# Kernel tuning notes

Measured on AMD Instinct MI355X. Metric: run time of the kernel, lower is better.

Reference implementation:

```python
import jax, jax.numpy as jnp
import numpy as np

B, N, K, M = 4, 32768, 128, 1024
C_IN, C_OUT, C_ATT, H = 256, 256, 256, 8
G = 32  # GroupNorm groups
EPS = 1e-6


def heat_diffusion(x, mass, evals, evecs, t):
    # to_basis: evecs^T @ (mass * x)  -> [B,K,C]
    x_spec = jnp.einsum('bnk,bnc->bkc', evecs, x * mass[..., None])
    coefs = jnp.exp(-evals[..., None] * t[None, None, :])  # [B,K,C]
    # from_basis: evecs @ spec -> [B,N,C]
    return jnp.einsum('bnk,bkc->bnc', evecs, coefs * x_spec)


def setup_inputs() -> dict:
    key = jax.random.key(0)
    ks = jax.random.split(key, 16)
    x = jax.random.normal(ks[0], (B, N, C_IN), jnp.float32)
    mass = jax.random.uniform(ks[1], (B, N), jnp.float32, 0.1, 1.0)
    evals = jnp.sort(jax.random.uniform(ks[2], (B, K), jnp.float32, 0.0, 10.0), axis=-1)
    evecs = jax.random.normal(ks[3], (B, N, K), jnp.float32) / np.sqrt(N)
    # unique sorted farthest-point indices per mesh (equiv. to boolean mask with M True)
    far_idx = jnp.stack([jnp.sort(jax.random.permutation(jax.random.fold_in(ks[4], b), N)[:M])
                         for b in range(B)]).astype(jnp.int32)
    s = 1.0 / np.sqrt(C_IN)
    params = dict(
        diff_in_t=jnp.full((C_IN,), 0.01, jnp.float32),
        diff_out_t=jnp.full((C_OUT,), 0.01, jnp.float32),
        gn_w=jnp.ones((C_IN,), jnp.float32),
        gn_b=jnp.zeros((C_IN,), jnp.float32),
        Wq=jax.random.normal(ks[5], (C_IN, C_ATT), jnp.float32) * s,
        bq=jnp.zeros((C_ATT,), jnp.float32),
        Wk=jax.random.normal(ks[6], (C_IN, C_ATT), jnp.float32) * s,
        bk=jnp.zeros((C_ATT,), jnp.float32),
        Wv=jax.random.normal(ks[7], (C_IN, C_ATT), jnp.float32) * s,
        bv=jnp.zeros((C_ATT,), jnp.float32),
        Wo=jax.random.normal(ks[8], (C_ATT, C_OUT), jnp.float32) * s,
        bo=jnp.zeros((C_OUT,), jnp.float32),
        out_w=jnp.ones((C_OUT,), jnp.float32),
    )
    return dict(x=x, mass=mass, evals=evals, evecs=evecs, far_idx=far_idx, **params)


def reference(x, mass, evals, evecs, far_idx, diff_in_t, diff_out_t, gn_w, gn_b,
              Wq, bq, Wk, bk, Wv, bv, Wo, bo, out_w):
    # clamp (torch does this in-place under no_grad)
    diff_in_t = jnp.maximum(diff_in_t, 1e-8)
    diff_out_t = jnp.maximum(diff_out_t, 1e-8)
    out_w = jnp.maximum(out_w, 1e-8)

    x = heat_diffusion(x, mass, evals, evecs, diff_in_t)  # [B,N,C_IN]

    # masked gather of farthest points -> [B,M,C_IN]
    x_far = jnp.take_along_axis(x, far_idx[..., None], axis=1)

    # GroupNorm over (group-channels, points)
    xg = x_far.reshape(B, M, G, C_IN // G)
    mu = jnp.mean(xg, axis=(1, 3), keepdims=True)
    var = jnp.var(xg, axis=(1, 3), keepdims=True)
    xg = (xg - mu) * jax.lax.rsqrt(var + EPS)
    x_far = xg.reshape(B, M, C_IN) * gn_w + gn_b

    d = C_ATT // H
    q = (x_far @ Wq + bq).reshape(B, M, H, d)
    k = (x_far @ Wk + bk).reshape(B, M, H, d)
    v = (x_far @ Wv + bv).reshape(B, M, H, d)
    scores = jnp.einsum('bqhd,bkhd->bhqk', q, k) / np.sqrt(d)
    attn = jax.nn.softmax(scores, axis=-1)
    x_far = jnp.einsum('bhqk,bkhd->bqhd', attn, v).reshape(B, M, C_ATT)
    x_far = x_far @ Wo + bo  # [B,M,C_OUT]

    # scatter back into zeros at the farthest-point rows
    z = jnp.zeros((B, N, C_OUT), x.dtype)
    z = z.at[jnp.arange(B)[:, None], far_idx].set(x_far)

    out = heat_diffusion(z, mass, evals, evecs, diff_out_t)
    return out * out_w[None, None, :]
```

## Files before the change

kernel.cpp:

```cpp
#include <hip/hip_runtime.h>
#include <hip/hip_bf16.h>


#define Bn 4
#define Nn 32768
#define Kn 128
#define Cn 256
#define Mn 1024
#define Hn 8
#define Dn 32
#define NCH 64
#define MCH 16
#define SEG 8

typedef _Float16 f16;
typedef _Float16 f16x8 __attribute__((ext_vector_type(8)));
typedef float f32x4 __attribute__((ext_vector_type(4)));

__device__ __forceinline__ void gload_lds16(const float* g, float* l) {
    __builtin_amdgcn_global_load_lds(
        (const __attribute__((address_space(1))) void*)g,
        (__attribute__((address_space(3))) void*)l, 16, 0, 0);
}

__global__ __launch_bounds__(512) void k_tobasis1(
    const float* __restrict__ x, const float* __restrict__ mass,
    const float* __restrict__ evecs, float* __restrict__ part)
{
    const int nch = blockIdx.x, b = blockIdx.z;
    const int n0 = nch * (Nn / NCH);
    const int t = threadIdx.x;
    const int lane = t & 63, w = t >> 6;
    const int lr = lane & 15, lg = lane >> 4;
    const int wm = (w & 1) * 64;
    const int wc = (w >> 1) * 64;

    __shared__ float evS[32][128];
    __shared__ float xS[32][256];
    __shared__ __align__(16) f16 evH[128][40];
    __shared__ __align__(16) f16 evL[128][40];
    __shared__ __align__(16) f16 xH[256][40];
    __shared__ __align__(16) f16 xL[256][40];

    const size_t rb0 = (size_t)b * Nn + n0;

    f32x4 acc[4][4] = {};

    {
        const float* eb = evecs + rb0 * Kn;
        const float* xb = x + rb0 * Cn;
#pragma unroll
        for (int iw = 0; iw < 2; iw++) {
            const int sl = w * 2 + iw;
            gload_lds16(eb + sl * 256 + lane * 4, (float*)evS + sl * 256);
        }
#pragma unroll
        for (int iw = 0; iw < 4; iw++) {
            const int sl = w * 4 + iw;
            gload_lds16(xb + sl * 256 + lane * 4, (float*)xS + sl * 256);
        }
    }

    for (int s = 0; s < 16; s++) {
        asm volatile("s_waitcnt vmcnt(0)" ::: "memory");
        __builtin_amdgcn_s_barrier();

        {
            const int k = (w & 1) * 64 + lane;
            const int g = w >> 1;
            f16x8 hv, lv;
#pragma unroll
            for (int r = 0; r < 8; r++) {
                const float f = evS[g * 8 + r][k];
                const f16 h = (f16)f;
                hv[r] = h;
                lv[r] = (f16)(f - (float)h);
            }
            *(f16x8*)&evH[k][g * 8] = hv;
            *(f16x8*)&evL[k][g * 8] = lv;
        }
#pragma unroll
        for (int i = 0; i < 2; i++) {
            const int c = (w & 3) * 64 + lane;
            const int g = i * 2 + (w >> 2);
            const size_t rowb = rb0 + s * 32 + g * 8;
            f16x8 hv, lv;
#pragma unroll
            for (int r = 0; r < 8; r++) {
                const float f = xS[g * 8 + r][c] * mass[rowb + r];
                const f16 h = (f16)f;
                hv[r] = h;
                lv[r] = (f16)(f - (float)h);
            }
            *(f16x8*)&xH[c][g * 8] = hv;
            *(f16x8*)&xL[c][g * 8] = lv;
        }

        asm volatile("s_waitcnt lgkmcnt(0)" ::: "memory");
        __builtin_amdgcn_s_barrier();

        if (s < 15) {
            const float* eb = evecs + (rb0 + (size_t)(s + 1) * 32) * Kn;
            const float* xb = x + (rb0 + (size_t)(s + 1) * 32) * Cn;
#pragma unroll
            for (int iw = 0; iw < 2; iw++) {
                const int sl = w * 2 + iw;
                gload_lds16(eb + sl * 256 + lane * 4, (float*)evS + sl * 256);
            }
#pragma unroll
            for (int iw = 0; iw < 4; iw++) {
                const int sl = w * 4 + iw;
                gload_lds16(xb + sl * 256 + lane * 4, (float*)xS + sl * 256);
            }
        }

        f16x8 aH[4], aL[4], bH[4], bL[4];
#pragma unroll
        for (int i = 0; i < 4; i++) {
            aH[i] = *(const f16x8*)&evH[wm + i * 16 + lr][lg * 8];
            aL[i] = *(const f16x8*)&evL[wm + i * 16 + lr][lg * 8];
            bH[i] = *(const f16x8*)&xH[wc + i * 16 + lr][lg * 8];
            bL[i] = *(const f16x8*)&xL[wc + i * 16 + lr][lg * 8];
        }
#pragma unroll
        for (int i = 0; i < 4; i++)
#pragma unroll
            for (int j = 0; j < 4; j++) {
                acc[i][j] = __builtin_amdgcn_mfma_f32_16x16x32_f16(aH[i], bH[j], acc[i][j], 0, 0, 0);
                acc[i][j] = __builtin_amdgcn_mfma_f32_16x16x32_f16(aH[i], bL[j], acc[i][j], 0, 0, 0);
                acc[i][j] = __builtin_amdgcn_mfma_f32_16x16x32_f16(aL[i], bH[j], acc[i][j], 0, 0, 0);
            }
    }

    float* dst = part + ((size_t)b * NCH + nch) * (Kn * Cn);
#pragma unroll
    for (int i = 0; i < 4; i++)
#pragma unroll
        for (int j = 0; j < 4; j++) {
            const int m0 = wm + i * 16 + lg * 4;
            const int c = wc + j * 16 + lr;
#pragma unroll
            for (int r = 0; r < 4; r++)
                dst[(size_t)(m0 + r) * Cn + c] = acc[i][j][r];
        }
}

__global__ __launch_bounds__(256) void k_reduce(
    const float* __restrict__ part, int nchunks,
    const float* __restrict__ evals, const float* __restrict__ tvec,
    float* __restrict__ spec)
{
    const int b = blockIdx.x >> 7, k = blockIdx.x & 127, c = threadIdx.x;
    float ssum = 0.f;
    const float* p = part + ((size_t)b * nchunks * Kn + k) * Cn + c;
    for (int j = 0; j < nchunks; j++) ssum += p[(size_t)j * Kn * Cn];
    const float lam = evals[b * Kn + k];
    const float tt = fmaxf(tvec[c], 1e-8f);
    spec[((size_t)b * Kn + k) * Cn + c] = ssum * __expf(-lam * tt);
}

__global__ __launch_bounds__(128) void k_gather(
    const float* __restrict__ evecs, const float* __restrict__ mass,
    const int* __restrict__ far, float* __restrict__ evf, float* __restrict__ massf)
{
    const int row = blockIdx.x;
    const int b = row >> 10;
    const int idx = far[row];
    const int t = threadIdx.x;
    evf[(size_t)row * Kn + t] = evecs[((size_t)b * Nn + idx) * Kn + t];
    if (t == 0) massf[row] = mass[(size_t)b * Nn + idx];
}

struct G3 {
    const float* W[3];
    const float* bias[3];
    float* out[3];
};

template<int KD, bool PERB, bool MMASS>
__global__ __launch_bounds__(256) void k_gemm64(
    const float* __restrict__ X, G3 g, const float* __restrict__ massf)
{
    const int mt = blockIdx.x, ct = blockIdx.y, z = blockIdx.z;
    const int row0 = mt * 64, c0 = ct * 64;
    const int b = row0 >> 10;
    const float* Wp = g.W[z];
    const float* bias = g.bias[z];
    float* out = g.out[z];
    const size_t woff = PERB ? (size_t)b * KD * 256 : 0;

    __shared__ float xT[32][68];
    __shared__ float wl[32][64];
    const int t = threadIdx.x, tx = t & 15, ty = t >> 4;
    float acc[4][4] = {};

    for (int k0 = 0; k0 < KD; k0 += 32) {
        {
            const int m = t >> 2, cc0 = (t & 3) * 8;
            const float* xs = X + (size_t)(row0 + m) * KD + k0 + cc0;
            float4 a0 = *(const float4*)xs, a1 = *(const float4*)(xs + 4);
            xT[cc0 + 0][m] = a0.x; xT[cc0 + 1][m] = a0.y; xT[cc0 + 2][m] = a0.z; xT[cc0 + 3][m] = a0.w;
            xT[cc0 + 4][m] = a1.x; xT[cc0 + 5][m] = a1.y; xT[cc0 + 6][m] = a1.z; xT[cc0 + 7][m] = a1.w;
        }
        {
            const int cc = t >> 3, col = (t & 7) * 8;
            const float* wsrc = Wp + woff + (size_t)(k0 + cc) * 256 + c0 + col;
            float4 a0 = *(const float4*)wsrc, a1 = *(const float4*)(wsrc + 4);
            wl[cc][col + 0] = a0.x; wl[cc][col + 1] = a0.y; wl[cc][col + 2] = a0.z; wl[cc][col + 3] = a0.w;
            wl[cc][col + 4] = a1.x; wl[cc][col + 5] = a1.y; wl[cc][col + 6] = a1.z; wl[cc][col + 7] = a1.w;
        }
        __syncthreads();
#pragma unroll 8
        for (int cc = 0; cc < 32; cc++) {
            float4 xv = *(const float4*)&xT[cc][ty * 4];
            float4 wv = *(const float4*)&wl[cc][tx * 4];
            float xa[4] = {xv.x, xv.y, xv.z, xv.w};
            float wa[4] = {wv.x, wv.y, wv.z, wv.w};
#pragma unroll
            for (int i = 0; i < 4; i++)
#pragma unroll
                for (int j = 0; j < 4; j++) acc[i][j] += xa[i] * wa[j];
        }
        __syncthreads();
    }
    float bj[4] = {0.f, 0.f, 0.f, 0.f};
    if (bias) {
#pragma unroll
        for (int j = 0; j < 4; j++) bj[j] = bias[c0 + tx * 4 + j];
    }
#pragma unroll
    for (int i = 0; i < 4; i++) {
        const int row = row0 + ty * 4 + i;
        const float mm = MMASS ? massf[row] : 1.f;
        *(float4*)(out + (size_t)row * 256 + c0 + tx * 4) =
            make_float4((acc[i][0] + bj[0]) * mm, (acc[i][1] + bj[1]) * mm,
                        (acc[i][2] + bj[2]) * mm, (acc[i][3] + bj[3]) * mm);
    }
}

__global__ __launch_bounds__(256) void k_gnstats(const float* __restrict__ xfar, float* __restrict__ gst)
{
    const int b = blockIdx.x >> 5, g = blockIdx.x & 31;
    const int t = threadIdx.x;
    float s = 0.f, s2 = 0.f;
#pragma unroll
    for (int i = 0; i < 4; i++) {
        const int m = t * 4 + i;
        const float* p = xfar + ((size_t)b * Mn + m) * Cn + g * 8;
        float4 a = *(const float4*)p;
        float4 c = *(const float4*)(p + 4);
        s += a.x + a.y + a.z + a.w + c.x + c.y + c.z + c.w;
        s2 += a.x * a.x + a.y * a.y + a.z * a.z + a.w * a.w +
              c.x * c.x + c.y * c.y + c.z * c.z + c.w * c.w;
    }
    __shared__ float sb[256], sb2[256];
    sb[t] = s; sb2[t] = s2;
    __syncthreads();
    for (int o = 128; o > 0; o >>= 1) {
        if (t < o) { sb[t] += sb[t + o]; sb2[t] += sb2[t + o]; }
        __syncthreads();
    }
    if (t == 0) {
        const float mean = sb[0] * (1.f / 8192.f);
        const float var = sb2[0] * (1.f / 8192.f) - mean * mean;
        gst[2 * blockIdx.x] = mean;
        gst[2 * blockIdx.x + 1] = rsqrtf(var + 1e-6f);
    }
}

__global__ __launch_bounds__(256) void k_gnapply(
    const float* __restrict__ xfar, const float* __restrict__ gst,
    const float* __restrict__ gw, const float* __restrict__ gb, float* __restrict__ xn)
{
    const int idx = (blockIdx.x * 256 + threadIdx.x) * 4;
    const int c = idx & 255;
    const int row = idx >> 8;
    const int b = row >> 10;
    const int g = c >> 3;
    const float2 st = *(const float2*)&gst[2 * (b * 32 + g)];
    float4 vv = *(const float4*)&xfar[idx];
    float4 w4 = *(const float4*)&gw[c];
    float4 b4 = *(const float4*)&gb[c];
    float4 o;
    o.x = (vv.x - st.x) * st.y * w4.x + b4.x;
    o.y = (vv.y - st.x) * st.y * w4.y + b4.y;
    o.z = (vv.z - st.x) * st.y * w4.z + b4.z;
    o.w = (vv.w - st.x) * st.y * w4.w + b4.w;
    *(float4*)&xn[idx] = o;
}

__global__ __launch_bounds__(256) void k_attn(
    const float* __restrict__ q, const float* __restrict__ kbuf, const float* __restrict__ vbuf,
    float* __restrict__ pacc, float* __restrict__ pm, float* __restrict__ pl)
{
    const int qt = blockIdx.x;
    const int seg = blockIdx.y;
    const int bh = blockIdx.z;
    const int b = bh >> 3, h = bh & 7;
    const int t = threadIdx.x;
    const int tx = t & 15, ty = t >> 4;

    __shared__ float qT[32][68];
    __shared__ float kT[32][68];
    __shared__ float vsm[64][36];
    __shared__ float psT[64][72];
    __shared__ float red[64][16];

    const int q0 = qt * 64;
    {
        const int row = t >> 2, d0 = (t & 3) * 8;
        const float* qp = q + ((size_t)b * Mn + q0 + row) * Cn + h * Dn + d0;
        float4 a0 = *(const float4*)qp, a1 = *(const float4*)(qp + 4);
        qT[d0 + 0][row] = a0.x; qT[d0 + 1][row] = a0.y; qT[d0 + 2][row] = a0.z; qT[d0 + 3][row] = a0.w;
        qT[d0 + 4][row] = a1.x; qT[d0 + 5][row] = a1.y; qT[d0 + 6][row] = a1.z; qT[d0 + 7][row] = a1.w;
    }

    const float scale = 0.17677669529663687f;
    float m_i[4], l_i[4], acc[4][2];
#pragma unroll
    for (int i = 0; i < 4; i++) { m_i[i] = -1e30f; l_i[i] = 0.f; acc[i][0] = 0.f; acc[i][1] = 0.f; }

    for (int kt = 0; kt < 2; kt++) {
        __syncthreads();
        {
            const int row = t >> 2, d0 = (t & 3) * 8;
            const int k0 = seg * 128 + kt * 64;
            const float* kp = kbuf + ((size_t)b * Mn + k0 + row) * Cn + h * Dn + d0;
            float4 a0 = *(const float4*)kp, a1 = *(const float4*)(kp + 4);
            kT[d0 + 0][row] = a0.x; kT[d0 + 1][row] = a0.y; kT[d0 + 2][row] = a0.z; kT[d0 + 3][row] = a0.w;
            kT[d0 + 4][row] = a1.x; kT[d0 + 5][row] = a1.y; kT[d0 + 6][row] = a1.z; kT[d0 + 7][row] = a1.w;
            const float* vp = vbuf + ((size_t)b * Mn + k0 + row) * Cn + h * Dn + d0;
            *(float4*)&vsm[row][d0] = *(const float4*)vp;
            *(float4*)&vsm[row][d0 + 4] = *(const float4*)(vp + 4);
        }
        __syncthreads();

        float s[4][4] = {};
#pragma unroll 8
        for (int d = 0; d < 32; d++) {
            float4 qv = *(const float4*)&qT[d][ty * 4];
            float4 kv = *(const float4*)&kT[d][tx * 4];
            float qa[4] = {qv.x, qv.y, qv.z, qv.w};
            float ka[4] = {kv.x, kv.y, kv.z, kv.w};
#pragma unroll
            for (int i = 0; i < 4; i++)
#pragma unroll
                for (int j = 0; j < 4; j++) s[i][j] += qa[i] * ka[j];
        }
        float tmax[4];
#pragma unroll
        for (int i = 0; i < 4; i++) {
            s[i][0] *= scale; s[i][1] *= scale; s[i][2] *= scale; s[i][3] *= scale;
            tmax[i] = fmaxf(fmaxf(s[i][0], s[i][1]), fmaxf(s[i][2], s[i][3]));
        }
#pragma unroll
        for (int i = 0; i < 4; i++) red[ty * 4 + i][tx] = tmax[i];
        __syncthreads();
        float nm[4];
#pragma unroll
        for (int i = 0; i < 4; i++) {
            const int row = ty * 4 + i;
            float mx = m_i[i];
#pragma unroll
            for (int xj = 0; xj < 16; xj++) mx = fmaxf(mx, red[row][xj]);
            nm[i] = mx;
        }
        __syncthreads();
        float tsum[4];
#pragma unroll
        for (int i = 0; i < 4; i++) {
            float p0 = __expf(s[i][0] - nm[i]);
            float p1 = __expf(s[i][1] - nm[i]);
            float p2 = __expf(s[i][2] - nm[i]);
            float p3 = __expf(s[i][3] - nm[i]);
            s[i][0] = p0; s[i][1] = p1; s[i][2] = p2; s[i][3] = p3;
            tsum[i] = p0 + p1 + p2 + p3;
        }
#pragma unroll
        for (int kk = 0; kk < 4; kk++)
            *(float4*)&psT[tx * 4 + kk][ty * 4] = make_float4(s[0][kk], s[1][kk], s[2][kk], s[3][kk]);
#pragma unroll
        for (int i = 0; i < 4; i++) red[ty * 4 + i][tx] = tsum[i];
        __syncthreads();
#pragma unroll
        for (int i = 0; i < 4; i++) {
            const int row = ty * 4 + i;
            float rs = 0.f;
#pragma unroll
            for (int xj = 0; xj < 16; xj++) rs += red[row][xj];
            const float r = __expf(m_i[i] - nm[i]);
            l_i[i] = l_i[i] * r + rs;
            m_i[i] = nm[i];
            acc[i][0] *= r; acc[i][1] *= r;
        }
#pragma unroll 8
        for (int k = 0; k < 64; k++) {
            float4 pv = *(const float4*)&psT[k][ty * 4];
            float2 vv = *(const float2*)&vsm[k][tx * 2];
            acc[0][0] += pv.x * vv.x; acc[0][1] += pv.x * vv.y;
            acc[1][0] += pv.y * vv.x; acc[1][1] += pv.y * vv.y;
            acc[2][0] += pv.z * vv.x; acc[2][1] += pv.z * vv.y;
            acc[3][0] += pv.w * vv.x; acc[3][1] += pv.w * vv.y;
        }
    }
#pragma unroll
    for (int i = 0; i < 4; i++) {
        const int m = q0 + ty * 4 + i;
        const size_t pr = (((size_t)seg * Bn + b) * Hn + h) * Mn + m;
        if (tx == 0) { pm[pr] = m_i[i]; pl[pr] = l_i[i]; }
        *(float2*)(pacc + pr * 32 + tx * 2) = make_float2(acc[i][0], acc[i][1]);
    }
}

__global__ __launch_bounds__(256) void k_comb(
    const float* __restrict__ pacc, const float* __restrict__ pm, const float* __restrict__ pl,
    float* __restrict__ att)
{
    const int t = threadIdx.x;
    const size_t row = (size_t)blockIdx.x * 8 + (t >> 5);
    const int j = t & 31;
    float M = -1e30f;
#pragma unroll
    for (int s = 0; s < SEG; s++) M = fmaxf(M, pm[(size_t)s * 32768 + row]);
    float L = 0.f, a = 0.f;
#pragma unroll
    for (int s = 0; s < SEG; s++) {
        const float w = __expf(pm[(size_t)s * 32768 + row] - M);
        L += w * pl[(size_t)s * 32768 + row];
        a += w * pacc[((size_t)s * 32768 + row) * 32 + j];
    }
    const int bh = (int)(row >> 10);
    const int mrow = (int)(row & 1023);
    const int b = bh >> 3, h = bh & 7;
    att[((size_t)b * Mn + mrow) * Cn + h * 32 + j] = a / L;
}

__global__ __launch_bounds__(256) void k_tobasis2(
    const float* __restrict__ evf, const float* __restrict__ xo, float* __restrict__ part)
{
    const int mch = blockIdx.x, ct = blockIdx.y, b = blockIdx.z;
    const int m0 = mch * (Mn / MCH);
    const int c0 = ct * 128;
    __shared__ float ev[32][128];
    __shared__ float xm[32][128];
    const int t = threadIdx.x, tx = t & 15, ty = t >> 4;
    float acc[8][8];
#pragma unroll
    for (int i = 0; i < 8; i++)
#pragma unroll
        for (int j = 0; j < 8; j++) acc[i][j] = 0.f;
    const int lr = t >> 3, lc = (t & 7) * 16;
    for (int s = 0; s < Mn / MCH; s += 32) {
        const size_t mrow = (size_t)b * Mn + m0 + s + lr;
        {
            const float* es = evf + mrow * Kn + lc;
            *(float4*)&ev[lr][lc]      = *(const float4*)es;
            *(float4*)&ev[lr][lc + 4]  = *(const float4*)(es + 4);
            *(float4*)&ev[lr][lc + 8]  = *(const float4*)(es + 8);
            *(float4*)&ev[lr][lc + 12] = *(const float4*)(es + 12);
            const float* xs = xo + mrow * Cn + c0 + lc;
            *(float4*)&xm[lr][lc]      = *(const float4*)xs;
            *(float4*)&xm[lr][lc + 4]  = *(const float4*)(xs + 4);
            *(float4*)&xm[lr][lc + 8]  = *(const float4*)(xs + 8);
            *(float4*)&xm[lr][lc + 12] = *(const float4*)(xs + 12);
        }
        __syncthreads();
#pragma unroll 4
        for (int nn = 0; nn < 32; nn++) {
            float4 e0 = *(const float4*)&ev[nn][ty * 4];
            float4 e1 = *(const float4*)&ev[nn][64 + ty * 4];
            float4 x0 = *(const float4*)&xm[nn][tx * 4];
            float4 x1 = *(const float4*)&xm[nn][64 + tx * 4];
            float ee[8] = {e0.x, e0.y, e0.z, e0.w, e1.x, e1.y, e1.z, e1.w};
            float xx[8] = {x0.x, x0.y, x0.z, x0.w, x1.x, x1.y, x1.z, x1.w};
#pragma unroll
            for (int i = 0; i < 8; i++)
#pragma unroll
                for (int j = 0; j < 8; j++) acc[i][j] += ee[i] * xx[j];
        }
        __syncthreads();
    }
    float* dst = part + ((size_t)b * MCH + mch) * (Kn * Cn);
#pragma unroll
    for (int i = 0; i < 8; i++) {
        const int k = (i < 4) ? (ty * 4 + i) : (64 + ty * 4 + i - 4);
        *(float4*)(dst + (size_t)k * Cn + c0 + tx * 4) =
            make_float4(acc[i][0], acc[i][1], acc[i][2], acc[i][3]);
        *(float4*)(dst + (size_t)k * Cn + c0 + 64 + tx * 4) =
            make_float4(acc[i][4], acc[i][5], acc[i][6], acc[i][7]);
    }
}

__global__ __launch_bounds__(256) void k_frombasis2(
    const float* __restrict__ evecs, const float* __restrict__ spec,
    const float* __restrict__ outw, float* __restrict__ out)
{
    const int nt = blockIdx.x, ct = blockIdx.y, b = blockIdx.z;
    const int n0 = nt * 128, c0 = ct * 128;
    __shared__ float evT[32][132];
    __shared__ float sp[32][128];
    const int t = threadIdx.x, tx = t & 15, ty = t >> 4;
    float acc[8][8];
#pragma unroll
    for (int i = 0; i < 8; i++)
#pragma unroll
        for (int j = 0; j < 8; j++) acc[i][j] = 0.f;
    const int en = t >> 1, ek0 = (t & 1) * 16;
    const int sr = t >> 3, sc = (t & 7) * 16;
    for (int k0 = 0; k0 < Kn; k0 += 32) {
        {
            const float* es = evecs + ((size_t)b * Nn + n0 + en) * Kn + k0 + ek0;
            float4 a0 = *(const float4*)es, a1 = *(const float4*)(es + 4);
            float4 a2 = *(const float4*)(es + 8), a3 = *(const float4*)(es + 12);
            evT[ek0 + 0][en] = a0.x; evT[ek0 + 1][en] = a0.y; evT[ek0 + 2][en] = a0.z; evT[ek0 + 3][en] = a0.w;
            evT[ek0 + 4][en] = a1.x; evT[ek0 + 5][en] = a1.y; evT[ek0 + 6][en] = a1.z; evT[ek0 + 7][en] = a1.w;
            evT[ek0 + 8][en] = a2.x; evT[ek0 + 9][en] = a2.y; evT[ek0 + 10][en] = a2.z; evT[ek0 + 11][en] = a2.w;
            evT[ek0 + 12][en] = a3.x; evT[ek0 + 13][en] = a3.y; evT[ek0 + 14][en] = a3.z; evT[ek0 + 15][en] = a3.w;
            const float* ss = spec + ((size_t)b * Kn + k0 + sr) * Cn + c0 + sc;
            *(float4*)&sp[sr][sc]      = *(const float4*)ss;
            *(float4*)&sp[sr][sc + 4]  = *(const float4*)(ss + 4);
            *(float4*)&sp[sr][sc + 8]  = *(const float4*)(ss + 8);
            *(float4*)&sp[sr][sc + 12] = *(const float4*)(ss + 12);
        }
        __syncthreads();
#pragma unroll 4
        for (int kk2 = 0; kk2 < 32; kk2++) {
            float4 e0 = *(const float4*)&evT[kk2][ty * 4];
            float4 e1 = *(const float4*)&evT[kk2][64 + ty * 4];
            float4 s0 = *(const float4*)&sp[kk2][tx * 4];
            float4 s1 = *(const float4*)&sp[kk2][64 + tx * 4];
            float ee[8] = {e0.x, e0.y, e0.z, e0.w, e1.x, e1.y, e1.z, e1.w};
            float sv[8] = {s0.x, s0.y, s0.z, s0.w, s1.x, s1.y, s1.z, s1.w};
#pragma unroll
            for (int i = 0; i < 8; i++)
#pragma unroll
                for (int j = 0; j < 8; j++) acc[i][j] += ee[i] * sv[j];
        }
        __syncthreads();
    }
    float ow[8];
#pragma unroll
    for (int j = 0; j < 8; j++) {
        const int c = c0 + ((j < 4) ? (tx * 4 + j) : (64 + tx * 4 + j - 4));
        ow[j] = fmaxf(outw[c], 1e-8f);
    }
#pragma unroll
    for (int i = 0; i < 8; i++) {
        const int n = n0 + ((i < 4) ? (ty * 4 + i) : (64 + ty * 4 + i - 4));
        float* od = out + ((size_t)b * Nn + n) * Cn + c0;
        *(float4*)(od + tx * 4) =
            make_float4(acc[i][0] * ow[0], acc[i][1] * ow[1], acc[i][2] * ow[2], acc[i][3] * ow[3]);
        *(float4*)(od + 64 + tx * 4) =
            make_float4(acc[i][4] * ow[4], acc[i][5] * ow[5], acc[i][6] * ow[6], acc[i][7] * ow[7]);
    }
}

extern "C" void kernel_launch(void* const* d_in, const int* in_sizes, int n_in,
                              void* d_out, int out_size, void* d_ws, size_t ws_size,
                              hipStream_t stream)
{
    const float* x     = (const float*)d_in[0];
    const float* mass  = (const float*)d_in[1];
    const float* evals = (const float*)d_in[2];
    const float* evecs = (const float*)d_in[3];
    const int*   far   = (const int*)d_in[4];
    const float* t_in  = (const float*)d_in[5];
    const float* t_out = (const float*)d_in[6];
    const float* gn_w  = (const float*)d_in[7];
    const float* gn_b  = (const float*)d_in[8];
    const float* Wq    = (const float*)d_in[9];
    const float* bq    = (const float*)d_in[10];
    const float* Wk    = (const float*)d_in[11];
    const float* bk    = (const float*)d_in[12];
    const float* Wv    = (const float*)d_in[13];
    const float* bv    = (const float*)d_in[14];
    const float* Wo    = (const float*)d_in[15];
    const float* bo    = (const float*)d_in[16];
    const float* outw  = (const float*)d_in[17];
    float* out = (float*)d_out;
    float* ws = (float*)d_ws;

    float* A     = ws;
    float* evf   = ws    + 8388608;
    float* massf = evf   + 524288;
    float* gst   = massf + 4096;
    float* pm    = gst   + 256;
    float* pl    = pm    + 262144;
    float* spec1 = pl    + 262144;
    float* xfar  = spec1 + 131072;
    float* xn    = xfar  + 1048576;
    float* q     = xn    + 1048576;
    float* kk    = q     + 1048576;
    float* v     = kk    + 1048576;
    float* pacc  = A;
    float* part2 = A;
    float* spec2 = spec1;
    float* xo    = xfar;
    float* att   = xn;

    k_tobasis1<<<dim3(NCH, 1, Bn), 512, 0, stream>>>(x, mass, evecs, A);
    k_reduce<<<Bn * Kn, Cn, 0, stream>>>(A, NCH, evals, t_in, spec1);
    k_gather<<<Bn * Mn, Kn, 0, stream>>>(evecs, mass, far, evf, massf);
    {
        G3 g{};
        g.W[0] = spec1; g.bias[0] = nullptr; g.out[0] = xfar;
        k_gemm64<128, true, false><<<dim3(64, 4, 1), 256, 0, stream>>>(evf, g, nullptr);
    }
    k_gnstats<<<Bn * 32, 256, 0, stream>>>(xfar, gst);
    k_gnapply<<<1024, 256, 0, stream>>>(xfar, gst, gn_w, gn_b, xn);
    {
        G3 g{};
        g.W[0] = Wq; g.W[1] = Wk; g.W[2] = Wv;
        g.bias[0] = bq; g.bias[1] = bk; g.bias[2] = bv;
        g.out[0] = q; g.out[1] = kk; g.out[2] = v;
        k_gemm64<256, false, false><<<dim3(64, 4, 3), 256, 0, stream>>>(xn, g, nullptr);
    }
    k_attn<<<dim3(16, SEG, 32), 256, 0, stream>>>(q, kk, v, pacc, pm, pl);
    k_comb<<<4096, 256, 0, stream>>>(pacc, pm, pl, att);
    {
        G3 g{};
        g.W[0] = Wo; g.bias[0] = bo; g.out[0] = xo;
        k_gemm64<256, false, true><<<dim3(64, 4, 1), 256, 0, stream>>>(att, g, massf);
    }
    k_tobasis2<<<dim3(MCH, 2, Bn), 256, 0, stream>>>(evf, xo, part2);
    k_reduce<<<Bn * Kn, Cn, 0, stream>>>(part2, MCH, evals, t_out, spec2);
    k_frombasis2<<<dim3(256, 2, Bn), 256, 0, stream>>>(evecs, spec2, outw, out);
}
```

Measured before the change: 628.9 us.

## Double-buffer staging in to-basis kernel, swizzle f16 split tiles, stage mass in LDS

```diff
diff --git a/kernel.cpp b/kernel.cpp
--- a/kernel.cpp
+++ b/kernel.cpp
@@ -35,92 +35,96 @@
     const int wm = (w & 1) * 64;
     const int wc = (w >> 1) * 64;
 
-    __shared__ float evS[32][128];
-    __shared__ float xS[32][256];
-    __shared__ __align__(16) f16 evH[128][40];
-    __shared__ __align__(16) f16 evL[128][40];
-    __shared__ __align__(16) f16 xH[256][40];
-    __shared__ __align__(16) f16 xL[256][40];
+    __shared__ __align__(16) float evS[2][32][128];
+    __shared__ __align__(16) float xS[2][32][256];
+    __shared__ __align__(16) f16 evT[128][64];
+    __shared__ __align__(16) f16 xT[256][64];
+    __shared__ __align__(16) float massS[512];
 
     const size_t rb0 = (size_t)b * Nn + n0;
+    const float* ebase = evecs + rb0 * Kn;
+    const float* xbase = x + rb0 * Cn;
 
     f32x4 acc[4][4] = {};
 
-    {
-        const float* eb = evecs + rb0 * Kn;
-        const float* xb = x + rb0 * Cn;
-#pragma unroll
-        for (int iw = 0; iw < 2; iw++) {
-            const int sl = w * 2 + iw;
-            gload_lds16(eb + sl * 256 + lane * 4, (float*)evS + sl * 256);
-        }
-#pragma unroll
-        for (int iw = 0; iw < 4; iw++) {
-            const int sl = w * 4 + iw;
-            gload_lds16(xb + sl * 256 + lane * 4, (float*)xS + sl * 256);
-        }
+    if (w < 2) gload_lds16(mass + rb0 + w * 256 + lane * 4, massS + w * 256);
+#pragma unroll
+    for (int ss = 0; ss < 2; ss++) {
+        const float* eb = ebase + (size_t)ss * 32 * Kn;
+        const float* xb = xbase + (size_t)ss * 32 * Cn;
+#pragma unroll
+        for (int iw = 0; iw < 2; iw++)
+            gload_lds16(eb + (w * 2 + iw) * 256 + lane * 4, &evS[ss][0][0] + (w * 2 + iw) * 256);
+#pragma unroll
+        for (int iw = 0; iw < 4; iw++)
+            gload_lds16(xb + (w * 4 + iw) * 256 + lane * 4, &xS[ss][0][0] + (w * 4 + iw) * 256);
     }
 
     for (int s = 0; s < 16; s++) {
-        asm volatile("s_waitcnt vmcnt(0)" ::: "memory");
+        const int p = s & 1;
+        if (s == 15) { asm volatile("s_waitcnt vmcnt(0)" ::: "memory"); }
+        else         { asm volatile("s_waitcnt vmcnt(6)" ::: "memory"); }
+        __builtin_amdgcn_sched_barrier(0);
         __builtin_amdgcn_s_barrier();
 
         {
-            const int k = (w & 1) * 64 + lane;
-            const int g = w >> 1;
+            const int k = t & 127;
+            const int g = t >> 7;
             f16x8 hv, lv;
 #pragma unroll
             for (int r = 0; r < 8; r++) {
-                const float f = evS[g * 8 + r][k];
+                const float f = evS[p][g * 8 + r][k];
                 const f16 h = (f16)f;
                 hv[r] = h;
                 lv[r] = (f16)(f - (float)h);
             }
-            *(f16x8*)&evH[k][g * 8] = hv;
-            *(f16x8*)&evL[k][g * 8] = lv;
-        }
-#pragma unroll
-        for (int i = 0; i < 2; i++) {
-            const int c = (w & 3) * 64 + lane;
-            const int g = i * 2 + (w >> 2);
-            const size_t rowb = rb0 + s * 32 + g * 8;
-            f16x8 hv, lv;
-#pragma unroll
-            for (int r = 0; r < 8; r++) {
-                const float f = xS[g * 8 + r][c] * mass[rowb + r];
-                const f16 h = (f16)f;
-                hv[r] = h;
-                lv[r] = (f16)(f - (float)h);
+            *(f16x8*)&evT[k][((g) ^ (k & 7)) * 8] = hv;
+            *(f16x8*)&evT[k][((4 + g) ^ (k & 7)) * 8] = lv;
+        }
+        {
+            const int c = t & 255;
+            const int g2 = t >> 8;
+#pragma unroll
+            for (int jj = 0; jj < 2; jj++) {
+                const int ch = g2 * 2 + jj;
+                f16x8 hv, lv;
+#pragma unroll
+                for (int r = 0; r < 8; r++) {
+                    const int n = ch * 8 + r;
+                    const float f = xS[p][n][c] * massS[s * 32 + n];
+                    const f16 h = (f16)f;
+                    hv[r] = h;
+                    lv[r] = (f16)(f - (float)h);
+                }
+                *(f16x8*)&xT[c][((ch) ^ (c & 7)) * 8] = hv;
+                *(f16x8*)&xT[c][((4 + ch) ^ (c & 7)) * 8] = lv;
             }
-            *(f16x8*)&xH[c][g * 8] = hv;
-            *(f16x8*)&xL[c][g * 8] = lv;
         }
 
         asm volatile("s_waitcnt lgkmcnt(0)" ::: "memory");
+        __builtin_amdgcn_sched_barrier(0);
         __builtin_amdgcn_s_barrier();
 
-        if (s < 15) {
-            const float* eb = evecs + (rb0 + (size_t)(s + 1) * 32) * Kn;
-            const float* xb = x + (rb0 + (size_t)(s + 1) * 32) * Cn;
-#pragma unroll
-            for (int iw = 0; iw < 2; iw++) {
-                const int sl = w * 2 + iw;
-                gload_lds16(eb + sl * 256 + lane * 4, (float*)evS + sl * 256);
-            }
-#pragma unroll
-            for (int iw = 0; iw < 4; iw++) {
-                const int sl = w * 4 + iw;
-                gload_lds16(xb + sl * 256 + lane * 4, (float*)xS + sl * 256);
-            }
+        if (s + 2 < 16) {
+            const float* eb = ebase + (size_t)(s + 2) * 32 * Kn;
+            const float* xb = xbase + (size_t)(s + 2) * 32 * Cn;
+#pragma unroll
+            for (int iw = 0; iw < 2; iw++)
+                gload_lds16(eb + (w * 2 + iw) * 256 + lane * 4, &evS[p][0][0] + (w * 2 + iw) * 256);
+#pragma unroll
+            for (int iw = 0; iw < 4; iw++)
+                gload_lds16(xb + (w * 4 + iw) * 256 + lane * 4, &xS[p][0][0] + (w * 4 + iw) * 256);
         }
 
         f16x8 aH[4], aL[4], bH[4], bL[4];
 #pragma unroll
         for (int i = 0; i < 4; i++) {
-            aH[i] = *(const f16x8*)&evH[wm + i * 16 + lr][lg * 8];
-            aL[i] = *(const f16x8*)&evL[wm + i * 16 + lr][lg * 8];
-            bH[i] = *(const f16x8*)&xH[wc + i * 16 + lr][lg * 8];
-            bL[i] = *(const f16x8*)&xL[wc + i * 16 + lr][lg * 8];
+            const int rk = wm + i * 16 + lr;
+            aH[i] = *(const f16x8*)&evT[rk][((lg) ^ (rk & 7)) * 8];
+            aL[i] = *(const f16x8*)&evT[rk][((4 + lg) ^ (rk & 7)) * 8];
+            const int rc = wc + i * 16 + lr;
+            bH[i] = *(const f16x8*)&xT[rc][((lg) ^ (rc & 7)) * 8];
+            bL[i] = *(const f16x8*)&xT[rc][((4 + lg) ^ (rc & 7)) * 8];
         }
 #pragma unroll
         for (int i = 0; i < 4; i++)
```

After: 600.7 us. 1.05x faster.
